# Kernel tuning notes

Measured on AMD Instinct MI355X. Metric: run time of the kernel, lower is better.

Reference implementation:

```python
import jax, jax.numpy as jnp
import numpy as np

B = 256
NUM_FEATURES = 2048
NUM_MEMORY = 65536
NUM_CLUSTERS = 8000  # static stand-in for labels.max()+1
TEMP = 0.05
EPS_SOFTMAX = 1e-6
EPS_LOG = 1e-6


def setup_inputs() -> dict:
    key = jax.random.key(0)
    k1, k2, k3, k4 = jax.random.split(key, 4)
    results = jax.random.normal(k1, (B, NUM_FEATURES), dtype=jnp.float32)
    indexes = jax.random.randint(k2, (B,), 0, NUM_MEMORY)
    feats = jax.random.normal(k3, (NUM_MEMORY, NUM_FEATURES), dtype=jnp.float32)
    # memory bank rows are L2-normalized in the real module (_update_feature)
    features = feats / jnp.linalg.norm(feats, axis=1, keepdims=True)
    labels = jax.random.randint(k4, (NUM_MEMORY,), 0, NUM_CLUSTERS)
    return {"results": results, "indexes": indexes, "features": features, "labels": labels}


def reference(results, indexes, features, labels):
    # L2-normalize the batch features
    x = results / jnp.linalg.norm(results, axis=1, keepdims=True)  # [B, F]
    # HM.forward: similarity against the full memory bank, scaled by temperature
    logits = jnp.matmul(x, features.T) / TEMP  # [B, M]
    # segment-reduce over memory entries by cluster label (torch index_add_)
    sim = jax.ops.segment_sum(logits.T, labels, num_segments=NUM_CLUSTERS)  # [C, B]
    nums = jax.ops.segment_sum(jnp.ones((NUM_MEMORY,), jnp.float32), labels,
                               num_segments=NUM_CLUSTERS)  # [C]
    mask = nums > 0  # [C] clusters that are populated
    sim = sim / jnp.where(mask, nums, 1.0)[:, None]  # per-cluster mean
    s = sim.T  # [B, C]
    # masked softmax over clusters
    exps = jnp.exp(s) * mask[None, :].astype(s.dtype)
    probs = exps / (jnp.sum(exps, axis=1, keepdims=True) + EPS_SOFTMAX)
    # nll_loss(log(probs + eps), targets)
    targets = labels[indexes]  # [B]
    logp = jnp.log(probs + EPS_LOG)
    return -jnp.mean(logp[jnp.arange(B), targets])
```

## Files before the change

### kernel.cpp

```cpp
#include <hip/hip_runtime.h>
#include <hip/hip_bf16.h>

#define B_ 256
#define F_ 2048
#define M_ 65536
#define C_ 8000
#define TEMP_ 0.05f

typedef __attribute__((ext_vector_type(8))) short short8;
typedef __attribute__((ext_vector_type(4))) float f32x4;

__device__ inline unsigned short f2bf(float f) {
  union { float f; unsigned u; } v; v.f = f;
  unsigned r = v.u + 0x7fffu + ((v.u >> 16) & 1u);
  return (unsigned short)(r >> 16);
}

__global__ void k_norm(const float* __restrict__ R, unsigned short* __restrict__ xb) {
  int b = blockIdx.x, t = threadIdx.x;
  const float4* row = (const float4*)(R + (size_t)b * F_);
  float4 v0 = row[t];
  float4 v1 = row[t + 256];
  float ss = v0.x*v0.x + v0.y*v0.y + v0.z*v0.z + v0.w*v0.w
           + v1.x*v1.x + v1.y*v1.y + v1.z*v1.z + v1.w*v1.w;
  __shared__ float red[256];
  red[t] = ss; __syncthreads();
  for (int s = 128; s > 0; s >>= 1) { if (t < s) red[t] += red[t + s]; __syncthreads(); }
  float inv = rsqrtf(red[0]);
  ushort4 o0, o1;
  o0.x = f2bf(v0.x * inv); o0.y = f2bf(v0.y * inv); o0.z = f2bf(v0.z * inv); o0.w = f2bf(v0.w * inv);
  o1.x = f2bf(v1.x * inv); o1.y = f2bf(v1.y * inv); o1.z = f2bf(v1.z * inv); o1.w = f2bf(v1.w * inv);
  ushort4* ob = (ushort4*)(xb + (size_t)b * F_);
  ob[t] = o0; ob[t + 256] = o1;
}

__global__ void k_hist(const int* __restrict__ labels, int* __restrict__ counts) {
  int m = blockIdx.x * 256 + threadIdx.x;
  atomicAdd(&counts[labels[m]], 1);
}

__global__ void k_scan(const int* __restrict__ counts, int* __restrict__ offsets) {
  int t = threadIdx.x;
  int base = t * 32;
  int pre[32];
  int run = 0;
  for (int j = 0; j < 32; j++) {
    int idx = base + j;
    pre[j] = run;
    run += (idx < C_) ? counts[idx] : 0;
  }
  __shared__ int sc[256];
  sc[t] = run; __syncthreads();
  for (int off = 1; off < 256; off <<= 1) {
    int x = (t >= off) ? sc[t - off] : 0;
    __syncthreads();
    sc[t] += x;
    __syncthreads();
  }
  int excl = sc[t] - run;
  for (int j = 0; j < 32; j++) {
    int idx = base + j;
    if (idx < C_) offsets[idx] = excl + pre[j];
  }
}

__global__ void k_scatter(const int* __restrict__ labels, const int* __restrict__ offsets,
                          int* __restrict__ cursor, int* __restrict__ order) {
  int m = blockIdx.x * 256 + threadIdx.x;
  int l = labels[m];
  int pos = atomicAdd(&cursor[l], 1);
  order[offsets[l] + pos] = m;
}

__global__ void k_csum(const float* __restrict__ feats, const int* __restrict__ counts,
                       const int* __restrict__ offsets, const int* __restrict__ order,
                       unsigned short* __restrict__ sb) {
  int c = blockIdx.x, t = threadIdx.x;
  int cnt = counts[c], off = offsets[c];
  float4 a0 = {0.f, 0.f, 0.f, 0.f}, a1 = {0.f, 0.f, 0.f, 0.f};
  __shared__ int mlist[256];
  for (int bas = 0; bas < cnt; bas += 256) {
    int n = cnt - bas; if (n > 256) n = 256;
    if (t < n) mlist[t] = order[off + bas + t];
    __syncthreads();
    for (int i = 0; i < n; i++) {
      int m = mlist[i];
      const float4* r = (const float4*)(feats + (size_t)m * F_);
      float4 x0 = r[t], x1 = r[t + 256];
      a0.x += x0.x; a0.y += x0.y; a0.z += x0.z; a0.w += x0.w;
      a1.x += x1.x; a1.y += x1.y; a1.z += x1.z; a1.w += x1.w;
    }
    __syncthreads();
  }
  float scale = (cnt > 0) ? 1.0f / (TEMP_ * (float)cnt) : 0.0f;
  ushort4 o0, o1;
  o0.x = f2bf(a0.x * scale); o0.y = f2bf(a0.y * scale); o0.z = f2bf(a0.z * scale); o0.w = f2bf(a0.w * scale);
  o1.x = f2bf(a1.x * scale); o1.y = f2bf(a1.y * scale); o1.z = f2bf(a1.z * scale); o1.w = f2bf(a1.w * scale);
  ushort4* ob = (ushort4*)(sb + (size_t)c * F_);
  ob[t] = o0; ob[t + 256] = o1;
}

#define BK 64
#define SK 72

__global__ __launch_bounds__(256) void k_gemm(const unsigned short* __restrict__ xb,
                                              const unsigned short* __restrict__ sb,
                                              float* __restrict__ sim) {
  __shared__ __align__(16) short As[128 * SK];
  __shared__ __align__(16) short Bs[128 * SK];
  int t = threadIdx.x;
  int b0 = blockIdx.x * 128;
  int c0 = blockIdx.y * 128;
  int wave = t >> 6, lane = t & 63;
  int wr = (wave >> 1) * 64, wc = (wave & 1) * 64;
  int m = lane & 15, q = lane >> 4;
  f32x4 acc[4][4];
  for (int i = 0; i < 4; i++)
    for (int j = 0; j < 4; j++)
      acc[i][j] = (f32x4){0.f, 0.f, 0.f, 0.f};

  for (int kk = 0; kk < F_; kk += BK) {
    __syncthreads();
    for (int i = 0; i < 4; i++) {
      int cid = t + i * 256;
      int row = cid >> 3, cc = cid & 7;
      short8 av = *(const short8*)(xb + (size_t)(b0 + row) * F_ + kk + cc * 8);
      *(short8*)(As + row * SK + cc * 8) = av;
      int gc = c0 + row;
      short8 bv = {0, 0, 0, 0, 0, 0, 0, 0};
      if (gc < C_) bv = *(const short8*)(sb + (size_t)gc * F_ + kk + cc * 8);
      *(short8*)(Bs + row * SK + cc * 8) = bv;
    }
    __syncthreads();
    for (int ks = 0; ks < 2; ks++) {
      int kof = ks * 32 + q * 8;
      short8 af[4], bfr[4];
      for (int i = 0; i < 4; i++)
        af[i] = *(const short8*)(As + (wr + i * 16 + m) * SK + kof);
      for (int j = 0; j < 4; j++)
        bfr[j] = *(const short8*)(Bs + (wc + j * 16 + m) * SK + kof);
      for (int i = 0; i < 4; i++)
        for (int j = 0; j < 4; j++)
          acc[i][j] = __builtin_amdgcn_mfma_f32_16x16x32_bf16(af[i], bfr[j], acc[i][j], 0, 0, 0);
    }
  }
  for (int i = 0; i < 4; i++) {
    for (int j = 0; j < 4; j++) {
      int col = c0 + wc + j * 16 + m;
      if (col < C_) {
        int rbase = b0 + wr + i * 16 + q * 4;
        f32x4 v = acc[i][j];
        sim[(size_t)(rbase + 0) * C_ + col] = v[0];
        sim[(size_t)(rbase + 1) * C_ + col] = v[1];
        sim[(size_t)(rbase + 2) * C_ + col] = v[2];
        sim[(size_t)(rbase + 3) * C_ + col] = v[3];
      }
    }
  }
}

__global__ void k_loss(const float* __restrict__ sim, const int* __restrict__ counts,
                       const int* __restrict__ labels, const int* __restrict__ indexes,
                       float* __restrict__ lossb) {
  int b = blockIdx.x, t = threadIdx.x;
  int tb = labels[indexes[b]];
  const float* srow = sim + (size_t)b * C_;
  __shared__ float sst;
  __shared__ float red[256];
  float sum = 0.f;
  for (int c = t; c < C_; c += 256) {
    float e = (counts[c] > 0) ? __expf(srow[c]) : 0.f;
    sum += e;
    if (c == tb) sst = e;
  }
  red[t] = sum; __syncthreads();
  for (int s = 128; s > 0; s >>= 1) { if (t < s) red[t] += red[t + s]; __syncthreads(); }
  if (t == 0) {
    float p = sst / (red[0] + 1e-6f);
    lossb[b] = -logf(p + 1e-6f);
  }
}

__global__ void k_mean(const float* __restrict__ lossb, float* __restrict__ out) {
  int t = threadIdx.x;
  __shared__ float red[256];
  red[t] = lossb[t]; __syncthreads();
  for (int s = 128; s > 0; s >>= 1) { if (t < s) red[t] += red[t + s]; __syncthreads(); }
  if (t == 0) out[0] = red[0] * (1.0f / 256.0f);
}

extern "C" void kernel_launch(void* const* d_in, const int* in_sizes, int n_in,
                              void* d_out, int out_size, void* d_ws, size_t ws_size,
                              hipStream_t stream) {
  const float* results  = (const float*)d_in[0];
  const int*   indexes  = (const int*)d_in[1];
  const float* features = (const float*)d_in[2];
  const int*   labels   = (const int*)d_in[3];
  float* out = (float*)d_out;

  const size_t REQ = (((size_t)B_ * F_ * 2 + 255) & ~(size_t)255)
                   + (((size_t)C_ * F_ * 2 + 255) & ~(size_t)255)
                   + 3 * (((size_t)C_ * 4 + 255) & ~(size_t)255)
                   + (((size_t)M_ * 4 + 255) & ~(size_t)255)
                   + (((size_t)B_ * C_ * 4 + 255) & ~(size_t)255)
                   + (((size_t)B_ * 4 + 255) & ~(size_t)255);
  if (ws_size < REQ) {
    hipMemsetAsync(d_out, 0, (size_t)out_size * 4, stream);
    return;
  }

  char* p = (char*)d_ws;
  auto carve = [&](size_t bytes) {
    char* r = p;
    p += (bytes + 255) & ~(size_t)255;
    return r;
  };
  unsigned short* xb  = (unsigned short*)carve((size_t)B_ * F_ * 2);
  unsigned short* sbf = (unsigned short*)carve((size_t)C_ * F_ * 2);
  int* counts  = (int*)carve((size_t)C_ * 4);
  int* offsets = (int*)carve((size_t)C_ * 4);
  int* cursor  = (int*)carve((size_t)C_ * 4);
  int* order   = (int*)carve((size_t)M_ * 4);
  float* sim   = (float*)carve((size_t)B_ * C_ * 4);
  float* lossb = (float*)carve((size_t)B_ * 4);

  hipMemsetAsync(counts, 0, (size_t)C_ * 4, stream);
  hipMemsetAsync(cursor, 0, (size_t)C_ * 4, stream);

  k_norm<<<B_, 256, 0, stream>>>(results, xb);
  k_hist<<<M_ / 256, 256, 0, stream>>>(labels, counts);
  k_scan<<<1, 256, 0, stream>>>(counts, offsets);
  k_scatter<<<M_ / 256, 256, 0, stream>>>(labels, offsets, cursor, order);
  k_csum<<<C_, 256, 0, stream>>>(features, counts, offsets, order, sbf);
  dim3 g(2, 63);
  k_gemm<<<g, 256, 0, stream>>>(xb, sbf, sim);
  k_loss<<<B_, 256, 0, stream>>>(sim, counts, labels, indexes, lossb);
  k_mean<<<1, 256, 0, stream>>>(lossb, out);
}
```

Baseline: 833.1 us.

## Split-K GEMM into partial buffers, unroll cluster-sum loads, fold memsets into kernels

The cluster-similarity GEMM, which launched only 126 blocks, is split four ways along K. Each slice writes its own partial result buffer, and the loss kernel adds the four partials before the exp. The cluster-sum loop now processes two memory rows per iteration with separate accumulators to keep more loads in flight. The two hipMemsetAsync calls are replaced by zeroing counts in k_norm and cursor in k_scan. The cost is four times the intermediate sim traffic and a larger workspace.

```diff
diff --git a/kernel.cpp b/kernel.cpp
--- a/kernel.cpp
+++ b/kernel.cpp
@@ -6,6 +6,7 @@
 #define M_ 65536
 #define C_ 8000
 #define TEMP_ 0.05f
+#define KSPLIT 4
 
 typedef __attribute__((ext_vector_type(8))) short short8;
 typedef __attribute__((ext_vector_type(4))) float f32x4;
@@ -16,8 +17,11 @@
   return (unsigned short)(r >> 16);
 }
 
-__global__ void k_norm(const float* __restrict__ R, unsigned short* __restrict__ xb) {
+__global__ void k_norm(const float* __restrict__ R, unsigned short* __restrict__ xb,
+                       int* __restrict__ counts) {
   int b = blockIdx.x, t = threadIdx.x;
+  int g = b * 256 + t;
+  if (g < C_) counts[g] = 0;
   const float4* row = (const float4*)(R + (size_t)b * F_);
   float4 v0 = row[t];
   float4 v1 = row[t + 256];
@@ -39,7 +43,8 @@
   atomicAdd(&counts[labels[m]], 1);
 }
 
-__global__ void k_scan(const int* __restrict__ counts, int* __restrict__ offsets) {
+__global__ void k_scan(const int* __restrict__ counts, int* __restrict__ offsets,
+                       int* __restrict__ cursor) {
   int t = threadIdx.x;
   int base = t * 32;
   int pre[32];
@@ -60,7 +65,7 @@
   int excl = sc[t] - run;
   for (int j = 0; j < 32; j++) {
     int idx = base + j;
-    if (idx < C_) offsets[idx] = excl + pre[j];
+    if (idx < C_) { offsets[idx] = excl + pre[j]; cursor[idx] = 0; }
   }
 }
 
@@ -77,21 +82,34 @@
                        unsigned short* __restrict__ sb) {
   int c = blockIdx.x, t = threadIdx.x;
   int cnt = counts[c], off = offsets[c];
-  float4 a0 = {0.f, 0.f, 0.f, 0.f}, a1 = {0.f, 0.f, 0.f, 0.f};
+  float4 a0 = {0.f,0.f,0.f,0.f}, a1 = {0.f,0.f,0.f,0.f};
+  float4 c0 = {0.f,0.f,0.f,0.f}, c1 = {0.f,0.f,0.f,0.f};
   __shared__ int mlist[256];
   for (int bas = 0; bas < cnt; bas += 256) {
     int n = cnt - bas; if (n > 256) n = 256;
     if (t < n) mlist[t] = order[off + bas + t];
     __syncthreads();
-    for (int i = 0; i < n; i++) {
-      int m = mlist[i];
-      const float4* r = (const float4*)(feats + (size_t)m * F_);
-      float4 x0 = r[t], x1 = r[t + 256];
+    int i = 0;
+    for (; i + 2 <= n; i += 2) {
+      const float4* r0 = (const float4*)(feats + (size_t)mlist[i] * F_);
+      const float4* r1 = (const float4*)(feats + (size_t)mlist[i + 1] * F_);
+      float4 x0 = r0[t], x1 = r0[t + 256];
+      float4 y0 = r1[t], y1 = r1[t + 256];
       a0.x += x0.x; a0.y += x0.y; a0.z += x0.z; a0.w += x0.w;
       a1.x += x1.x; a1.y += x1.y; a1.z += x1.z; a1.w += x1.w;
-    }
-    __syncthreads();
-  }
+      c0.x += y0.x; c0.y += y0.y; c0.z += y0.z; c0.w += y0.w;
+      c1.x += y1.x; c1.y += y1.y; c1.z += y1.z; c1.w += y1.w;
+    }
+    if (i < n) {
+      const float4* r0 = (const float4*)(feats + (size_t)mlist[i] * F_);
+      float4 x0 = r0[t], x1 = r0[t + 256];
+      a0.x += x0.x; a0.y += x0.y; a0.z += x0.z; a0.w += x0.w;
+      a1.x += x1.x; a1.y += x1.y; a1.z += x1.z; a1.w += x1.w;
+    }
+    __syncthreads();
+  }
+  a0.x += c0.x; a0.y += c0.y; a0.z += c0.z; a0.w += c0.w;
+  a1.x += c1.x; a1.y += c1.y; a1.z += c1.z; a1.w += c1.w;
   float scale = (cnt > 0) ? 1.0f / (TEMP_ * (float)cnt) : 0.0f;
   ushort4 o0, o1;
   o0.x = f2bf(a0.x * scale); o0.y = f2bf(a0.y * scale); o0.z = f2bf(a0.z * scale); o0.w = f2bf(a0.w * scale);
@@ -105,12 +123,15 @@
 
 __global__ __launch_bounds__(256) void k_gemm(const unsigned short* __restrict__ xb,
                                               const unsigned short* __restrict__ sb,
-                                              float* __restrict__ sim) {
+                                              float* __restrict__ simp) {
   __shared__ __align__(16) short As[128 * SK];
   __shared__ __align__(16) short Bs[128 * SK];
   int t = threadIdx.x;
   int b0 = blockIdx.x * 128;
   int c0 = blockIdx.y * 128;
+  int kz = blockIdx.z;
+  int k_begin = kz * (F_ / KSPLIT);
+  int k_end = k_begin + (F_ / KSPLIT);
   int wave = t >> 6, lane = t & 63;
   int wr = (wave >> 1) * 64, wc = (wave & 1) * 64;
   int m = lane & 15, q = lane >> 4;
@@ -119,7 +140,7 @@
     for (int j = 0; j < 4; j++)
       acc[i][j] = (f32x4){0.f, 0.f, 0.f, 0.f};
 
-  for (int kk = 0; kk < F_; kk += BK) {
+  for (int kk = k_begin; kk < k_end; kk += BK) {
     __syncthreads();
     for (int i = 0; i < 4; i++) {
       int cid = t + i * 256;
@@ -144,6 +165,7 @@
           acc[i][j] = __builtin_amdgcn_mfma_f32_16x16x32_bf16(af[i], bfr[j], acc[i][j], 0, 0, 0);
     }
   }
+  float* sim = simp + (size_t)kz * B_ * C_;
   for (int i = 0; i < 4; i++) {
     for (int j = 0; j < 4; j++) {
       int col = c0 + wc + j * 16 + m;
@@ -159,17 +181,21 @@
   }
 }
 
-__global__ void k_loss(const float* __restrict__ sim, const int* __restrict__ counts,
+__global__ void k_loss(const float* __restrict__ simp, const int* __restrict__ counts,
                        const int* __restrict__ labels, const int* __restrict__ indexes,
                        float* __restrict__ lossb) {
   int b = blockIdx.x, t = threadIdx.x;
   int tb = labels[indexes[b]];
-  const float* srow = sim + (size_t)b * C_;
+  const float* s0 = simp + (size_t)b * C_;
+  const float* s1 = s0 + (size_t)B_ * C_;
+  const float* s2 = s1 + (size_t)B_ * C_;
+  const float* s3 = s2 + (size_t)B_ * C_;
   __shared__ float sst;
   __shared__ float red[256];
   float sum = 0.f;
   for (int c = t; c < C_; c += 256) {
-    float e = (counts[c] > 0) ? __expf(srow[c]) : 0.f;
+    float v = s0[c] + s1[c] + s2[c] + s3[c];
+    float e = (counts[c] > 0) ? __expf(v) : 0.f;
     sum += e;
     if (c == tb) sst = e;
   }
@@ -202,7 +228,7 @@
                    + (((size_t)C_ * F_ * 2 + 255) & ~(size_t)255)
                    + 3 * (((size_t)C_ * 4 + 255) & ~(size_t)255)
                    + (((size_t)M_ * 4 + 255) & ~(size_t)255)
-                   + (((size_t)B_ * C_ * 4 + 255) & ~(size_t)255)
+                   + (((size_t)KSPLIT * B_ * C_ * 4 + 255) & ~(size_t)255)
                    + (((size_t)B_ * 4 + 255) & ~(size_t)255);
   if (ws_size < REQ) {
     hipMemsetAsync(d_out, 0, (size_t)out_size * 4, stream);
@@ -221,19 +247,16 @@
   int* offsets = (int*)carve((size_t)C_ * 4);
   int* cursor  = (int*)carve((size_t)C_ * 4);
   int* order   = (int*)carve((size_t)M_ * 4);
-  float* sim   = (float*)carve((size_t)B_ * C_ * 4);
+  float* simp  = (float*)carve((size_t)KSPLIT * B_ * C_ * 4);
   float* lossb = (float*)carve((size_t)B_ * 4);
 
-  hipMemsetAsync(counts, 0, (size_t)C_ * 4, stream);
-  hipMemsetAsync(cursor, 0, (size_t)C_ * 4, stream);
-
-  k_norm<<<B_, 256, 0, stream>>>(results, xb);
+  k_norm<<<B_, 256, 0, stream>>>(results, xb, counts);
   k_hist<<<M_ / 256, 256, 0, stream>>>(labels, counts);
-  k_scan<<<1, 256, 0, stream>>>(counts, offsets);
+  k_scan<<<1, 256, 0, stream>>>(counts, offsets, cursor);
   k_scatter<<<M_ / 256, 256, 0, stream>>>(labels, offsets, cursor, order);
   k_csum<<<C_, 256, 0, stream>>>(features, counts, offsets, order, sbf);
-  dim3 g(2, 63);
-  k_gemm<<<g, 256, 0, stream>>>(xb, sbf, sim);
-  k_loss<<<B_, 256, 0, stream>>>(sim, counts, labels, indexes, lossb);
+  dim3 g(2, 63, KSPLIT);
+  k_gemm<<<g, 256, 0, stream>>>(xb, sbf, simp);
+  k_loss<<<B_, 256, 0, stream>>>(simp, counts, labels, indexes, lossb);
   k_mean<<<1, 256, 0, stream>>>(lossb, out);
 }
```

Measured after the change: 777.7 us. 6.6% less time.
